# Kernel tuning notes

Hardware: AMD Instinct MI355X
Metric: run time of the kernel (lower is better)

The kernel has to match this reference:

```python
import jax, jax.numpy as jnp
import numpy as np

WINDOW_SIZE = 11
SIGMA = 1.5
C1 = 0.01 ** 2
C2 = 0.03 ** 2


def _make_window(channel, dtype=jnp.float32):
    # Faithful to torch `gaussian`: center at window_size/2 (= 5.5 for ws=11)
    x = np.arange(WINDOW_SIZE, dtype=np.float64)
    g = np.exp(-((x - WINDOW_SIZE / 2) ** 2) / (2.0 * SIGMA ** 2))
    g = (g / g.sum()).astype(np.float32)
    w2d = np.outer(g, g)  # (ws, ws)
    w = np.broadcast_to(w2d, (channel, 1, WINDOW_SIZE, WINDOW_SIZE)).copy()
    return jnp.asarray(w, dtype=dtype)


def _dwconv(x, w, channel):
    pad = WINDOW_SIZE // 2
    return jax.lax.conv_general_dilated(
        x, w,
        window_strides=(1, 1),
        padding=[(pad, pad), (pad, pad)],
        dimension_numbers=("NCHW", "OIHW", "NCHW"),
        feature_group_count=channel,
    )


def setup_inputs() -> dict:
    key = jax.random.key(0)
    k1, k2 = jax.random.split(key)
    B, C, H, W = 16, 3, 512, 512
    img1 = jax.random.uniform(k1, (B, C, H, W), dtype=jnp.float32)
    img2 = jax.random.uniform(k2, (B, C, H, W), dtype=jnp.float32)
    return {"img1": img1, "img2": img2}


def reference(img1, img2):
    channel = img1.shape[1]
    window = _make_window(channel, img1.dtype)

    mu1 = _dwconv(img1, window, channel)
    mu2 = _dwconv(img2, window, channel)
    mu1_sq = mu1 * mu1
    mu2_sq = mu2 * mu2
    mu1_mu2 = mu1 * mu2

    sigma1_sq = _dwconv(img1 * img1, window, channel) - mu1_sq
    sigma2_sq = _dwconv(img2 * img2, window, channel) - mu2_sq
    sigma12 = _dwconv(img1 * img2, window, channel) - mu1_mu2

    numerator = (2 * mu1_mu2 + C1) * (2 * sigma12 + C2)
    denominator = (mu1_sq + mu2_sq + C1) * (sigma1_sq + sigma2_sq + C2)
    ssim_map = numerator / denominator
    return jnp.mean(ssim_map)  # size_average=True
```

## Files before the change

kernel.cpp:

```cpp
#include <hip/hip_runtime.h>
#include <cmath>


#define IMG_H 512
#define IMG_W 512
#define STRIPE 32
#define NSTR (IMG_H / STRIPE)
#define NPLANES 48
#define NBLOCKS (NPLANES * NSTR)
#define SSIM_C1 (0.01f * 0.01f)
#define SSIM_C2 (0.03f * 0.03f)

typedef float f32x2 __attribute__((ext_vector_type(2)));

struct W2x11 { float2 w[11]; };

__launch_bounds__(512, 2)
__global__ void ssim_main(const float* __restrict__ img1,
                          const float* __restrict__ img2,
                          float* __restrict__ blockSums, W2x11 wv) {
    __shared__ __align__(16) float2 abL[2][2][532];
    __shared__ __align__(16) float2 spL[2][2][532];
    __shared__ float red[8];

    const int x = threadIdx.x;
    const int bid = blockIdx.x;
    const int plane = bid >> 4;
    const int stripe = bid & (NSTR - 1);
    const int y0 = stripe * STRIPE;
    const size_t base = (size_t)plane * (IMG_H * IMG_W);

    if (x < 10) {
        const int col = (x < 5) ? x : (x + 512);
#pragma unroll
        for (int d = 0; d < 2; ++d)
#pragma unroll
            for (int r = 0; r < 2; ++r) {
                abL[d][r][col] = make_float2(0.f, 0.f);
                spL[d][r][col] = make_float2(0.f, 0.f);
            }
    }

    f32x2 rAB[11], rSP[11];
    float acc = 0.f;

    float pa0 = 0.f, pb0 = 0.f, pa1 = 0.f, pb1 = 0.f;
    {
        const int r0 = y0 - 5, r1 = y0 - 4;
        if (r0 >= 0) {
            pa0 = img1[base + (size_t)r0 * IMG_W + x];
            pb0 = img2[base + (size_t)r0 * IMG_W + x];
        }
        if (r1 >= 0) {
            pa1 = img1[base + (size_t)r1 * IMG_W + x];
            pb1 = img2[base + (size_t)r1 * IMG_W + x];
        }
    }

    int buf = 0;
#pragma unroll 1
    for (int c = 0; c < 2; ++c) {
#pragma unroll
        for (int jp = 0; jp < 11; ++jp) {
            const int p = c * 11 + jp;
            if (p < 21) {
                const int j1 = (2 * jp) % 11;
                const int j2 = (2 * jp + 1) % 11;
                {
                    f32x2 ab; ab.x = pa0; ab.y = pb0;
                    f32x2 sp;
                    sp.x = fmaf(pb0, pb0, pa0 * pa0);
                    sp.y = pa0 * pb0;
                    rAB[j1] = ab; rSP[j1] = sp;
                }
                if (p >= 5) {
                    f32x2 vAB = {0.f, 0.f}, vSP = {0.f, 0.f};
#pragma unroll
                    for (int k = 0; k < 11; ++k) {
                        const int s = (2 * jp + 1 + k) % 11;
                        f32x2 w2; w2.x = wv.w[k].x; w2.y = wv.w[k].y;
                        vAB = __builtin_elementwise_fma(w2, rAB[s], vAB);
                        vSP = __builtin_elementwise_fma(w2, rSP[s], vSP);
                    }
                    abL[buf][0][x + 5] = make_float2(vAB.x, vAB.y);
                    spL[buf][0][x + 5] = make_float2(vSP.x, vSP.y);
                }
                {
                    f32x2 ab; ab.x = pa1; ab.y = pb1;
                    f32x2 sp;
                    sp.x = fmaf(pb1, pb1, pa1 * pa1);
                    sp.y = pa1 * pb1;
                    rAB[j2] = ab; rSP[j2] = sp;
                }
                if (p >= 5) {
                    f32x2 vAB = {0.f, 0.f}, vSP = {0.f, 0.f};
#pragma unroll
                    for (int k = 0; k < 11; ++k) {
                        const int s = (2 * jp + 2 + k) % 11;
                        f32x2 w2; w2.x = wv.w[k].x; w2.y = wv.w[k].y;
                        vAB = __builtin_elementwise_fma(w2, rAB[s], vAB);
                        vSP = __builtin_elementwise_fma(w2, rSP[s], vSP);
                    }
                    abL[buf][1][x + 5] = make_float2(vAB.x, vAB.y);
                    spL[buf][1][x + 5] = make_float2(vSP.x, vSP.y);
                }
                pa0 = 0.f; pb0 = 0.f; pa1 = 0.f; pb1 = 0.f;
                if (p + 1 < 21) {
                    const int rn0 = y0 - 5 + 2 * p + 2;
                    const int rn1 = rn0 + 1;
                    if (rn0 >= 0 && rn0 < IMG_H) {
                        pa0 = img1[base + (size_t)rn0 * IMG_W + x];
                        pb0 = img2[base + (size_t)rn0 * IMG_W + x];
                    }
                    if (rn1 >= 0 && rn1 < IMG_H) {
                        pa1 = img1[base + (size_t)rn1 * IMG_W + x];
                        pb1 = img2[base + (size_t)rn1 * IMG_W + x];
                    }
                }
                if (p >= 5) {
                    __syncthreads();
                    const int sel = x >> 8;
                    const int u = x & 255;
                    const float2* Ap = abL[buf][sel];
                    const float2* Sp = spL[buf][sel];
                    f32x2 hAB0 = {0.f, 0.f}, hAB1 = {0.f, 0.f};
                    f32x2 hSP0 = {0.f, 0.f}, hSP1 = {0.f, 0.f};
#pragma unroll
                    for (int m = 0; m < 6; ++m) {
                        const float4 q = *(const float4*)(&Ap[2 * u + 2 * m]);
                        f32x2 lo; lo.x = q.x; lo.y = q.y;
                        f32x2 hi; hi.x = q.z; hi.y = q.w;
                        f32x2 w2;
                        w2.x = wv.w[2 * m].x; w2.y = wv.w[2 * m].y;
                        hAB0 = __builtin_elementwise_fma(w2, lo, hAB0);
                        hAB1 = __builtin_elementwise_fma(w2, hi, hAB1);
                        if (2 * m + 1 <= 10) {
                            w2.x = wv.w[2 * m + 1].x; w2.y = wv.w[2 * m + 1].y;
                            hAB0 = __builtin_elementwise_fma(w2, hi, hAB0);
                        }
                        if (2 * m - 1 >= 0) {
                            w2.x = wv.w[2 * m - 1].x; w2.y = wv.w[2 * m - 1].y;
                            hAB1 = __builtin_elementwise_fma(w2, lo, hAB1);
                        }
                    }
#pragma unroll
                    for (int m = 0; m < 6; ++m) {
                        const float4 q = *(const float4*)(&Sp[2 * u + 2 * m]);
                        f32x2 lo; lo.x = q.x; lo.y = q.y;
                        f32x2 hi; hi.x = q.z; hi.y = q.w;
                        f32x2 w2;
                        w2.x = wv.w[2 * m].x; w2.y = wv.w[2 * m].y;
                        hSP0 = __builtin_elementwise_fma(w2, lo, hSP0);
                        hSP1 = __builtin_elementwise_fma(w2, hi, hSP1);
                        if (2 * m + 1 <= 10) {
                            w2.x = wv.w[2 * m + 1].x; w2.y = wv.w[2 * m + 1].y;
                            hSP0 = __builtin_elementwise_fma(w2, hi, hSP0);
                        }
                        if (2 * m - 1 >= 0) {
                            w2.x = wv.w[2 * m - 1].x; w2.y = wv.w[2 * m - 1].y;
                            hSP1 = __builtin_elementwise_fma(w2, lo, hSP1);
                        }
                    }
                    {
                        const float vA = hAB0.x, vB = hAB0.y;
                        const float vS = hSP0.x, vP = hSP0.y;
                        const float mu11 = vA * vA, mu22 = vB * vB;
                        const float mu12 = vA * vB;
                        const float num = fmaf(2.f, mu12, SSIM_C1) *
                                          fmaf(2.f, vP - mu12, SSIM_C2);
                        const float d1  = mu11 + mu22;
                        const float den = (d1 + SSIM_C1) * ((vS - d1) + SSIM_C2);
                        acc = fmaf(num, __builtin_amdgcn_rcpf(den), acc);
                    }
                    {
                        const float vA = hAB1.x, vB = hAB1.y;
                        const float vS = hSP1.x, vP = hSP1.y;
                        const float mu11 = vA * vA, mu22 = vB * vB;
                        const float mu12 = vA * vB;
                        const float num = fmaf(2.f, mu12, SSIM_C1) *
                                          fmaf(2.f, vP - mu12, SSIM_C2);
                        const float d1  = mu11 + mu22;
                        const float den = (d1 + SSIM_C1) * ((vS - d1) + SSIM_C2);
                        acc = fmaf(num, __builtin_amdgcn_rcpf(den), acc);
                    }
                    buf ^= 1;
                }
            }
        }
    }

#pragma unroll
    for (int off = 32; off >= 1; off >>= 1)
        acc += __shfl_down(acc, off, 64);
    const int wave = x >> 6, lane = x & 63;
    if (lane == 0) red[wave] = acc;
    __syncthreads();
    if (x == 0) {
        float s = 0.f;
#pragma unroll
        for (int k = 0; k < 8; ++k) s += red[k];
        blockSums[bid] = s;
    }
}

__global__ void ssim_reduce(const float* __restrict__ bs,
                            float* __restrict__ out) {
    __shared__ double red[4];
    const int t = threadIdx.x;
    double a = 0.0;
    for (int idx = t; idx < NBLOCKS; idx += 256) a += (double)bs[idx];
#pragma unroll
    for (int off = 32; off >= 1; off >>= 1)
        a += __shfl_down(a, off, 64);
    const int wave = t >> 6, lane = t & 63;
    if (lane == 0) red[wave] = a;
    __syncthreads();
    if (t == 0) {
        const double s = red[0] + red[1] + red[2] + red[3];
        out[0] = (float)(s / (double)((double)NPLANES * IMG_H * IMG_W));
    }
}

extern "C" void kernel_launch(void* const* d_in, const int* in_sizes, int n_in,
                              void* d_out, int out_size, void* d_ws, size_t ws_size,
                              hipStream_t stream) {
    const float* img1 = (const float*)d_in[0];
    const float* img2 = (const float*)d_in[1];
    float* out = (float*)d_out;
    float* bs = (float*)d_ws;

    W2x11 wv;
    double g[11], s = 0.0;
    for (int i = 0; i < 11; ++i) {
        const double d = (double)i - 5.5;
        g[i] = exp(-(d * d) / (2.0 * 1.5 * 1.5));
        s += g[i];
    }
    for (int i = 0; i < 11; ++i) {
        const float w = (float)(g[i] / s);
        wv.w[i] = make_float2(w, w);
    }

    ssim_main<<<NBLOCKS, 512, 0, stream>>>(img1, img2, bs, wv);
    ssim_reduce<<<1, 256, 0, stream>>>(bs, out);
}
```

Before: 159.9 us.

## Halve stripe height and recompute squares/products on the fly to cut registers

The stripe height drops from 32 to 16 rows, doubling the block count per plane, and the plane and stripe indexing is updated to match. The second register ring (squared sums and cross products) is removed; these terms are now recomputed from the raw pixel ring inside each vertical tap loop. The intent is to lower register pressure and raise parallelism. In exchange, each output row pays more halo rows (10 extra per 16 instead of per 32) and extra ALU work per tap.

```diff
diff --git a/kernel.cpp b/kernel.cpp
--- a/kernel.cpp
+++ b/kernel.cpp
@@ -4,10 +4,12 @@
 
 #define IMG_H 512
 #define IMG_W 512
-#define STRIPE 32
+#define STRIPE 16
 #define NSTR (IMG_H / STRIPE)
 #define NPLANES 48
 #define NBLOCKS (NPLANES * NSTR)
+#define SROWS (STRIPE + 10)
+#define NPAIRS (SROWS / 2)
 #define SSIM_C1 (0.01f * 0.01f)
 #define SSIM_C2 (0.03f * 0.03f)
 
@@ -19,13 +21,13 @@
 __global__ void ssim_main(const float* __restrict__ img1,
                           const float* __restrict__ img2,
                           float* __restrict__ blockSums, W2x11 wv) {
-    __shared__ __align__(16) float2 abL[2][2][532];
-    __shared__ __align__(16) float2 spL[2][2][532];
+    __shared__ __align__(16) float2 abL[2][2][528];
+    __shared__ __align__(16) float2 spL[2][2][528];
     __shared__ float red[8];
 
     const int x = threadIdx.x;
     const int bid = blockIdx.x;
-    const int plane = bid >> 4;
+    const int plane = bid >> 5;
     const int stripe = bid & (NSTR - 1);
     const int y0 = stripe * STRIPE;
     const size_t base = (size_t)plane * (IMG_H * IMG_W);
@@ -41,7 +43,7 @@
             }
     }
 
-    f32x2 rAB[11], rSP[11];
+    f32x2 rAB[11];
     float acc = 0.f;
 
     float pa0 = 0.f, pb0 = 0.f, pa1 = 0.f, pb1 = 0.f;
@@ -63,50 +65,52 @@
 #pragma unroll
         for (int jp = 0; jp < 11; ++jp) {
             const int p = c * 11 + jp;
-            if (p < 21) {
-                const int j1 = (2 * jp) % 11;
-                const int j2 = (2 * jp + 1) % 11;
+            if (p < NPAIRS) {
                 {
                     f32x2 ab; ab.x = pa0; ab.y = pb0;
-                    f32x2 sp;
-                    sp.x = fmaf(pb0, pb0, pa0 * pa0);
-                    sp.y = pa0 * pb0;
-                    rAB[j1] = ab; rSP[j1] = sp;
+                    rAB[(2 * jp) % 11] = ab;
                 }
                 if (p >= 5) {
-                    f32x2 vAB = {0.f, 0.f}, vSP = {0.f, 0.f};
+                    f32x2 vAB = {0.f, 0.f};
+                    float vS = 0.f, vP = 0.f;
 #pragma unroll
                     for (int k = 0; k < 11; ++k) {
                         const int s = (2 * jp + 1 + k) % 11;
+                        const f32x2 ab = rAB[s];
                         f32x2 w2; w2.x = wv.w[k].x; w2.y = wv.w[k].y;
-                        vAB = __builtin_elementwise_fma(w2, rAB[s], vAB);
-                        vSP = __builtin_elementwise_fma(w2, rSP[s], vSP);
+                        vAB = __builtin_elementwise_fma(w2, ab, vAB);
+                        const float sq = fmaf(ab.y, ab.y, ab.x * ab.x);
+                        const float pr = ab.x * ab.y;
+                        vS = fmaf(wv.w[k].x, sq, vS);
+                        vP = fmaf(wv.w[k].x, pr, vP);
                     }
                     abL[buf][0][x + 5] = make_float2(vAB.x, vAB.y);
-                    spL[buf][0][x + 5] = make_float2(vSP.x, vSP.y);
+                    spL[buf][0][x + 5] = make_float2(vS, vP);
                 }
                 {
                     f32x2 ab; ab.x = pa1; ab.y = pb1;
-                    f32x2 sp;
-                    sp.x = fmaf(pb1, pb1, pa1 * pa1);
-                    sp.y = pa1 * pb1;
-                    rAB[j2] = ab; rSP[j2] = sp;
+                    rAB[(2 * jp + 1) % 11] = ab;
                 }
                 if (p >= 5) {
-                    f32x2 vAB = {0.f, 0.f}, vSP = {0.f, 0.f};
+                    f32x2 vAB = {0.f, 0.f};
+                    float vS = 0.f, vP = 0.f;
 #pragma unroll
                     for (int k = 0; k < 11; ++k) {
                         const int s = (2 * jp + 2 + k) % 11;
+                        const f32x2 ab = rAB[s];
                         f32x2 w2; w2.x = wv.w[k].x; w2.y = wv.w[k].y;
-                        vAB = __builtin_elementwise_fma(w2, rAB[s], vAB);
-                        vSP = __builtin_elementwise_fma(w2, rSP[s], vSP);
+                        vAB = __builtin_elementwise_fma(w2, ab, vAB);
+                        const float sq = fmaf(ab.y, ab.y, ab.x * ab.x);
+                        const float pr = ab.x * ab.y;
+                        vS = fmaf(wv.w[k].x, sq, vS);
+                        vP = fmaf(wv.w[k].x, pr, vP);
                     }
                     abL[buf][1][x + 5] = make_float2(vAB.x, vAB.y);
-                    spL[buf][1][x + 5] = make_float2(vSP.x, vSP.y);
+                    spL[buf][1][x + 5] = make_float2(vS, vP);
                 }
                 pa0 = 0.f; pb0 = 0.f; pa1 = 0.f; pb1 = 0.f;
-                if (p + 1 < 21) {
-                    const int rn0 = y0 - 5 + 2 * p + 2;
+                if (p + 1 < NPAIRS) {
+                    const int rn0 = y0 - 5 + 2 * (p + 1);
                     const int rn1 = rn0 + 1;
                     if (rn0 >= 0 && rn0 < IMG_H) {
                         pa0 = img1[base + (size_t)rn0 * IMG_W + x];
```

Measured after the change: 161.7 us. About the same (+1.1%).
